# Performance work log

Hardware: AMD Instinct MI355X
Metric: run time of the kernel (lower is better)

The kernel has to match this reference:

```python
import jax, jax.numpy as jnp
import numpy as np

K_REGION = 32
C_CONTEXT = 128
CONF_THR = 0.5


def safe_normalize(x):
    return x / jnp.maximum(x.sum(axis=-1, keepdims=True), 1e-6)


def _geometry(mask_grid, h, w):
    # mask_grid: [B, K, h*w] -> per-mask bbox (x_min,y_min,x_max,y_max) + area, vectorized
    B, K, _ = mask_grid.shape
    m2 = mask_grid.reshape(B, K, h, w)
    present = m2 > 0.05
    rows = present.any(-1)  # [B,K,h]
    cols = present.any(-2)  # [B,K,w]
    yi = jnp.arange(h)
    xi = jnp.arange(w)
    y_min = jnp.min(jnp.where(rows, yi, h), axis=-1).astype(jnp.float32)
    y_max = jnp.max(jnp.where(rows, yi, -1), axis=-1).astype(jnp.float32)
    x_min = jnp.min(jnp.where(cols, xi, w), axis=-1).astype(jnp.float32)
    x_max = jnp.max(jnp.where(cols, xi, -1), axis=-1).astype(jnp.float32)
    hden = float(max(h - 1, 1))
    wden = float(max(w - 1, 1))
    area = present.astype(jnp.float32).mean(axis=(-1, -2))
    geom = jnp.stack([x_min / wden, y_min / hden, x_max / wden, y_max / hden, area], axis=-1)
    has_any = present.any(axis=(-1, -2))
    return jnp.where(has_any[..., None], geom, 0.0).astype(mask_grid.dtype)


def setup_inputs():
    key = jax.random.key(0)
    ks = jax.random.split(key, 16)
    B, N, D, M, Hm, Wm, Qd, Hd = 8, 576, 1024, 64, 384, 384, 4096, 1024
    inp = {}
    inp['patch_tokens'] = jax.random.normal(ks[0], (B, N, D), jnp.float32)
    inp['masks'] = jax.random.uniform(ks[1], (B, M, Hm, Wm), jnp.float32)
    inp['scores'] = jax.random.uniform(ks[2], (B, M), jnp.float32)
    inp['question_embed'] = jax.random.normal(ks[3], (B, Qd), jnp.float32)
    s = 0.02
    inp['W1'] = jax.random.normal(ks[4], (5, D), jnp.float32) * s
    inp['b1'] = jnp.zeros((D,), jnp.float32)
    inp['W2'] = jax.random.normal(ks[5], (D, D), jnp.float32) * s
    inp['b2'] = jnp.zeros((D,), jnp.float32)
    inp['Wv'] = jax.random.normal(ks[6], (D, Hd), jnp.float32) * s
    inp['bv'] = jnp.zeros((Hd,), jnp.float32)
    inp['Wp'] = jax.random.normal(ks[7], (1, Hd), jnp.float32) * s
    inp['bp'] = jnp.zeros((Hd,), jnp.float32)
    inp['Wq'] = jax.random.normal(ks[8], (Qd, Hd), jnp.float32) * s
    inp['bq'] = jnp.zeros((Hd,), jnp.float32)
    inp['Wo'] = jax.random.normal(ks[9], (Hd, 1), jnp.float32) * s
    inp['bo'] = jnp.zeros((1,), jnp.float32)
    inp['type_emb'] = jax.random.normal(ks[10], (3, D), jnp.float32) * s
    inp['patch_h'] = 24
    inp['patch_w'] = 24
    return inp


def reference(patch_tokens, masks, scores, question_embed, W1, b1, W2, b2,
              Wv, bv, Wp, bp, Wq, bq, Wo, bo, type_emb, patch_h, patch_w):
    B, N, D = patch_tokens.shape
    h, w = patch_h, patch_w
    M = masks.shape[1]

    grounding_valid = (masks.reshape(B, M, -1).sum(-1) > 0).any(-1)  # [B]

    order = jnp.argsort(-scores, axis=1)
    scores_s = jnp.take_along_axis(scores, order, axis=1)
    masks_s = jnp.take_along_axis(masks, order[:, :, None, None], axis=1)
    masks_k = masks_s[:, :K_REGION]
    scores_k = scores_s[:, :K_REGION]
    valid = scores_k >= CONF_THR
    masks_k = masks_k * valid[:, :, None, None].astype(masks_k.dtype)
    scores_k = jnp.where(valid, scores_k, 0.0)

    # MaskDownsampler: adaptive avg pool (exact: Hm,Wm divisible by h,w)
    Hm, Wm = masks_k.shape[-2:]
    fh, fw = Hm // h, Wm // w
    mg = masks_k.reshape(B, K_REGION, h, fh, w, fw).mean(axis=(3, 5)).reshape(B, K_REGION, h * w)

    uniform = jnp.full((B, K_REGION, N), 1.0 / N, dtype=patch_tokens.dtype)
    mg = jnp.where(grounding_valid[:, None, None], mg, uniform)
    scores_k = jnp.where(grounding_valid[:, None], scores_k, 1.0)

    # RegionPooler
    nm = safe_normalize(jnp.maximum(mg, 0.0))
    pooled = jnp.einsum('bkn,bnd->bkd', nm, patch_tokens)
    weighted = pooled * scores_k[..., None]
    geom = _geometry(mg, h, w)  # [B,K,5]
    g = jax.nn.silu(geom @ W1 + b1) @ W2 + b2
    region_tokens = weighted + g

    patch_prior = (mg * scores_k[..., None]).sum(axis=1)
    patch_prior = safe_normalize(jnp.maximum(patch_prior, 0.0))
    patch_prior = jnp.where(grounding_valid[:, None], patch_prior, jnp.full_like(patch_prior, 1.0 / N))

    # RoutingScorer
    hid = jnp.tanh(patch_tokens @ Wv + bv
                   + patch_prior[:, :, None] @ Wp + bp
                   + (question_embed @ Wq + bq)[:, None, :])
    routing_scores = (hid @ Wo + bo)[..., 0]  # [B,N]
    routing_weights = jax.nn.softmax(routing_scores, axis=-1)

    top_k = min(C_CONTEXT, N)
    _, sel_idx = jax.lax.top_k(routing_scores, top_k)
    context_tokens = jnp.take_along_axis(patch_tokens, sel_idx[:, :, None], axis=1)
    sel_mask = jnp.zeros((B, N), patch_tokens.dtype).at[jnp.arange(B)[:, None], sel_idx].set(1.0)

    # BackgroundPooler
    residual = jnp.maximum(1.0 - sel_mask, 0.0)
    residual = residual / jnp.maximum(residual.sum(-1, keepdims=True), 1e-6)
    bg = jnp.einsum('bn,bnd->bd', residual, patch_tokens)

    region_tokens = region_tokens + type_emb[0][None, None, :]
    context_tokens = context_tokens + type_emb[1][None, None, :]
    background_token = bg[:, None, :] + type_emb[2][None, None, :]
    visual_tokens = jnp.concatenate([region_tokens, context_tokens, background_token], axis=1)

    return (visual_tokens, region_tokens, context_tokens, background_token,
            patch_prior, routing_weights, sel_idx, grounding_valid)
```

## Files before the change

### kernel.cpp

```cpp
#include <hip/hip_runtime.h>
#include <math.h>

typedef long long I64;

#define NB    8
#define NTOK  576
#define DIM   1024
#define NMASK 64
#define HMASK 384
#define WMASK 384
#define QDIM  4096
#define HDIM  1024
#define KREG  32
#define CCTX  128
#define GH    24
#define GW    24
#define GNUM  576

#define OFF_VIS 0
#define OFF_REG 1318912
#define OFF_CTX 1581056
#define OFF_BG  2629632
#define OFF_PP  2637824
#define OFF_RW  2642432
#define OFF_SEL 2647040
#define OFF_GV  2648064

#define WS_BS   0
#define WS_NMAT 294912
#define WS_SCK  442368
#define WS_H1   442624
#define WS_Q    704768
#define WS_Q2   712960
#define WS_GV   721152
#define WS_PP   721160
#define WS_CS   725768
#define WS_RSP  733960

#define QBLK      256
#define BS_BLOCKS (NB * NMASK * 24)

__global__ __launch_bounds__(384) void k_bsq(const float* __restrict__ masks,
                                             const float* __restrict__ qe,
                                             const float* __restrict__ Wq,
                                             const float* __restrict__ bq,
                                             float* __restrict__ ws) {
  int gid = blockIdx.x;
  int t = threadIdx.x;
  __shared__ float shm[2048 + 6 * 64];
  if (gid >= QBLK) {
    int gid2 = gid - QBLK;
    int yband = gid2 % 24;
    int bm = gid2 / 24;
    float (*sm)[96] = (float(*)[96])shm;
    const float4* src = (const float4*)(masks + (I64)bm * (HMASK * WMASK) + (I64)yband * 16 * WMASK);
    float4 s4 = src[t];
    float4 v1 = src[t + 384];
    float4 v2 = src[t + 768];
    float4 v3 = src[t + 1152];
    s4.x += v1.x; s4.y += v1.y; s4.z += v1.z; s4.w += v1.w;
    s4.x += v2.x; s4.y += v2.y; s4.z += v2.z; s4.w += v2.w;
    s4.x += v3.x; s4.y += v3.y; s4.z += v3.z; s4.w += v3.w;
    float s = (s4.x + s4.y) + (s4.z + s4.w);
    sm[t / 96][t % 96] = s;
    __syncthreads();
    if (t < 24) {
      float tt = 0.f;
      #pragma unroll
      for (int rg = 0; rg < 4; ++rg)
        #pragma unroll
        for (int c = 0; c < 4; ++c) tt += sm[rg][t * 4 + c];
      ws[WS_BS + (I64)bm * GNUM + yband * 24 + t] = tt;
    }
  } else {
    int b = gid >> 5;
    int r = gid & 31;
    int qb = r >> 1;
    int ih = r & 1;
    int base = ih * 2048;
    float* qs = shm;
    float (*sp)[64] = (float(*)[64])(shm + 2048);
    {
      const float4* s4 = (const float4*)(qe + (I64)b * QDIM + base);
      float4 v = s4[t];
      *(float4*)&qs[t * 4] = v;
      if (t < 128) {
        float4 v2 = s4[t + 384];
        *(float4*)&qs[(t + 384) * 4] = v2;
      }
    }
    __syncthreads();
    int dl = t & 63, ig = t >> 6;
    int d = qb * 64 + dl;
    const float* wq = Wq + d;
    float a0 = 0.f, a1 = 0.f, a2 = 0.f, a3 = 0.f;
    float a4 = 0.f, a5 = 0.f, a6 = 0.f, a7 = 0.f;
    int i = ig;
    for (; i + 42 < 2048; i += 48) {
      a0 = fmaf(qs[i],      wq[(I64)(base + i) * HDIM],      a0);
      a1 = fmaf(qs[i + 6],  wq[(I64)(base + i + 6) * HDIM],  a1);
      a2 = fmaf(qs[i + 12], wq[(I64)(base + i + 12) * HDIM], a2);
      a3 = fmaf(qs[i + 18], wq[(I64)(base + i + 18) * HDIM], a3);
      a4 = fmaf(qs[i + 24], wq[(I64)(base + i + 24) * HDIM], a4);
      a5 = fmaf(qs[i + 30], wq[(I64)(base + i + 30) * HDIM], a5);
      a6 = fmaf(qs[i + 36], wq[(I64)(base + i + 36) * HDIM], a6);
      a7 = fmaf(qs[i + 42], wq[(I64)(base + i + 42) * HDIM], a7);
    }
    for (; i < 2048; i += 6)
      a0 = fmaf(qs[i], wq[(I64)(base + i) * HDIM], a0);
    sp[ig][dl] = ((a0 + a1) + (a2 + a3)) + ((a4 + a5) + (a6 + a7));
    __syncthreads();
    if (t < 64) {
      float s2 = ((sp[0][t] + sp[1][t]) + (sp[2][t] + sp[3][t])) + (sp[4][t] + sp[5][t]);
      int dd = qb * 64 + t;
      float outv = s2 + (ih ? 0.f : bq[dd]);
      ws[(ih ? WS_Q2 : WS_Q) + (I64)b * HDIM + dd] = outv;
    }
  }
}

#define MGPAD 580
__global__ __launch_bounds__(256) void k_perbatch(
    const float* __restrict__ bs, const float* __restrict__ scores,
    const float* __restrict__ W1, const float* __restrict__ b1,
    float* __restrict__ ws, float* __restrict__ out) {
  int b = blockIdx.x;
  int t = threadIdx.x;
  __shared__ float s_mg[KREG][MGPAD];
  __shared__ float s_sc[NMASK];
  __shared__ float s_msum[NMASK];
  __shared__ int   s_order[NMASK];
  __shared__ float s_sck[KREG];
  __shared__ int   s_valid[KREG];
  __shared__ int   s_midx[KREG];
  __shared__ float s_rowsum[KREG];
  __shared__ float s_pp[GNUM];
  __shared__ float s_geom[KREG][5];
  __shared__ float s_red[64];
  __shared__ int   s_gv;
  __shared__ float s_ppsum;

  {
    int m = t >> 2, q = t & 3;
    const float4* p = (const float4*)(bs + ((I64)b * NMASK + m) * GNUM) + q * 36;
    float s = 0.f;
    #pragma unroll 4
    for (int j = 0; j < 36; ++j) {
      float4 v = p[j];
      s += v.x; s += v.y; s += v.z; s += v.w;
    }
    s += __shfl_xor(s, 1);
    s += __shfl_xor(s, 2);
    if (q == 0) s_msum[m] = s;
  }
  if (t < NMASK) s_sc[t] = scores[b * NMASK + t];
  __syncthreads();
  if (t == 0) {
    int g = 0;
    for (int m = 0; m < NMASK; ++m) g |= (s_msum[m] > 0.f) ? 1 : 0;
    s_gv = g;
  }
  if (t < NMASK) {
    float v = s_sc[t];
    int r = 0;
    for (int j = 0; j < NMASK; ++j) {
      float vj = s_sc[j];
      r += (vj > v) || (vj == v && j < t);
    }
    s_order[r] = t;
  }
  __syncthreads();
  const int gv = s_gv;
  if (t < KREG) {
    int m = s_order[t];
    float sc = s_sc[m];
    int valid = (sc >= 0.5f) ? 1 : 0;
    s_midx[t] = m;
    s_valid[t] = valid;
    float sck = gv ? (valid ? sc : 0.f) : 1.f;
    s_sck[t] = sck;
    ws[WS_SCK + b * KREG + t] = sck;
  }
  __syncthreads();
  {
    int k = t >> 3, sub = t & 7;
    const float inv256 = 1.f / 256.f;
    const float invN = 1.f / 576.f;
    float scale = gv ? (s_valid[k] ? inv256 : 0.f) : 0.f;
    float addv  = gv ? 0.f : invN;
    const float4* src = (const float4*)(bs + ((I64)b * NMASK + s_midx[k]) * GNUM) + sub * 18;
    float* dst = &s_mg[k][sub * 72];
    #pragma unroll 3
    for (int j = 0; j < 18; ++j) {
      float4 v = src[j];
      v.x = v.x * scale + addv;
      v.y = v.y * scale + addv;
      v.z = v.z * scale + addv;
      v.w = v.w * scale + addv;
      *(float4*)(dst + j * 4) = v;
    }
  }
  __syncthreads();
  {
    int k = t >> 3, sub = t & 7;
    float part = 0.f;
    for (int n = sub; n < GNUM; n += 8) part += fmaxf(s_mg[k][n], 0.f);
    part += __shfl_xor(part, 1);
    part += __shfl_xor(part, 2);
    part += __shfl_xor(part, 4);
    if (sub == 0) s_rowsum[k] = part;
  }
  __syncthreads();
  for (int idx = t; idx < KREG * GNUM; idx += 256) {
    int k = idx / GNUM, n = idx - k * GNUM;
    float v = fmaxf(s_mg[k][n], 0.f);
    ws[WS_NMAT + ((I64)b * KREG + k) * GNUM + n] = v / fmaxf(s_rowsum[k], 1e-6f);
  }
  for (int n = t; n < GNUM; n += 256) {
    float raw = 0.f;
    #pragma unroll
    for (int k = 0; k < KREG; ++k) raw = fmaf(s_mg[k][n], s_sck[k], raw);
    s_pp[n] = fmaxf(raw, 0.f);
  }
  __syncthreads();
  if (t < 64) {
    float s = 0.f;
    for (int n = t; n < GNUM; n += 64) s += s_pp[n];
    s_red[t] = s;
  }
  __syncthreads();
  if (t == 0) {
    float s = 0.f;
    for (int i = 0; i < 64; ++i) s += s_red[i];
    s_ppsum = s;
  }
  __syncthreads();
  {
    const float invN = 1.f / 576.f;
    float den = fmaxf(s_ppsum, 1e-6f);
    for (int n = t; n < GNUM; n += 256) {
      float v = gv ? (s_pp[n] / den) : invN;
      ws[WS_PP + b * GNUM + n] = v;
      out[OFF_PP + b * GNUM + n] = v;
    }
  }
  {
    int k = t >> 3, sub = t & 7;
    unsigned colmask = 0u;
    int ymin = GH, ymax = -1, cnt = 0;
    #pragma unroll
    for (int yy = 0; yy < 3; ++yy) {
      int y = sub * 3 + yy;
      unsigned rowm = 0u;
      for (int x = 0; x < GW; ++x)
        if (s_mg[k][y * GW + x] > 0.05f) rowm |= (1u << x);
      if (rowm) { if (y < ymin) ymin = y; if (y > ymax) ymax = y; }
      colmask |= rowm;
      cnt += __popc(rowm);
    }
    #pragma unroll
    for (int off = 1; off < 8; off <<= 1) {
      colmask |= (unsigned)__shfl_xor((int)colmask, off);
      cnt += __shfl_xor(cnt, off);
      int o1 = __shfl_xor(ymin, off); ymin = (o1 < ymin) ? o1 : ymin;
      int o2 = __shfl_xor(ymax, off); ymax = (o2 > ymax) ? o2 : ymax;
    }
    if (sub == 0) {
      float g0, g1, g2, g3, g4;
      if (cnt > 0) {
        int xmin = __ffs(colmask) - 1;
        int xmax = 31 - __clz(colmask);
        g0 = (float)xmin / 23.f;
        g1 = (float)ymin / 23.f;
        g2 = (float)xmax / 23.f;
        g3 = (float)ymax / 23.f;
        g4 = (float)cnt / 576.f;
      } else { g0 = g1 = g2 = g3 = g4 = 0.f; }
      s_geom[k][0] = g0; s_geom[k][1] = g1; s_geom[k][2] = g2;
      s_geom[k][3] = g3; s_geom[k][4] = g4;
    }
  }
  __syncthreads();
  for (int idx = t; idx < KREG * HDIM; idx += 256) {
    int k = idx >> 10, j = idx & 1023;
    float x = 0.f;
    #pragma unroll
    for (int i = 0; i < 5; ++i) x += s_geom[k][i] * W1[i * HDIM + j];
    x += b1[j];
    float sg = 1.f / (1.f + expf(-x));
    ws[WS_H1 + ((I64)b * KREG + k) * HDIM + j] = x * sg;
  }
  if (t == 0) {
    float g = gv ? 1.f : 0.f;
    ws[WS_GV + b] = g;
    out[OFF_GV + b] = g;
  }
}

__global__ __launch_bounds__(512) void k_region(
    const float* __restrict__ pt, const float* __restrict__ W2,
    const float* __restrict__ b2, const float* __restrict__ te,
    float* __restrict__ ws, float* __restrict__ out) {
  int blk = blockIdx.x;
  int b = blk >> 6, kg = (blk >> 3) & 7, dg = blk & 7;
  int t = threadIdx.x;
  int dl = t & 127;
  int qh = t >> 7;
  int d = dg * 128 + dl;
  const float* nmb = ws + WS_NMAT + ((I64)b * KREG + kg * 4) * GNUM;
  const float* h1b = ws + WS_H1 + ((I64)b * KREG + kg * 4) * HDIM;
  float accP[4] = {0, 0, 0, 0};
  float accG[4] = {0, 0, 0, 0};
  float accS = 0.f;
  int n0 = qh * 144, n1 = n0 + 144;
  for (int n = n0; n < n1; ++n) {
    float p = pt[((I64)b * NTOK + n) * DIM + d];
    accS += p;
    #pragma unroll
    for (int kk = 0; kk < 4; ++kk)
      accP[kk] = fmaf(nmb[kk * GNUM + n], p, accP[kk]);
  }
  int j0 = qh * 256, j1 = j0 + 256;
  for (int j = j0; j < j1; ++j) {
    float wv = W2[(I64)j * DIM + d];
    #pragma unroll
    for (int kk = 0; kk < 4; ++kk)
      accG[kk] = fmaf(h1b[kk * HDIM + j], wv, accG[kk]);
  }
  __shared__ float cmbP[4][4][128];
  __shared__ float cmbG[4][4][128];
  __shared__ float cmbS[4][128];
  #pragma unroll
  for (int kk = 0; kk < 4; ++kk) {
    cmbP[qh][kk][dl] = accP[kk];
    cmbG[qh][kk][dl] = accG[kk];
  }
  cmbS[qh][dl] = accS;
  __syncthreads();
  if (qh == 0) {
    float bb = b2[d], t0 = te[d];
    #pragma unroll
    for (int kk = 0; kk < 4; ++kk) {
      int k = kg * 4 + kk;
      float P = (cmbP[0][kk][dl] + cmbP[1][kk][dl]) + (cmbP[2][kk][dl] + cmbP[3][kk][dl]);
      float G = (cmbG[0][kk][dl] + cmbG[1][kk][dl]) + (cmbG[2][kk][dl] + cmbG[3][kk][dl]);
      float val = P * ws[WS_SCK + b * KREG + k] + G + bb + t0;
      out[OFF_REG + ((I64)b * KREG + k) * DIM + d] = val;
      out[OFF_VIS + ((I64)b * 161 + k) * DIM + d] = val;
    }
    if (kg == 0)
      ws[WS_CS + (I64)b * DIM + d] =
          (cmbS[0][dl] + cmbS[1][dl]) + (cmbS[2][dl] + cmbS[3][dl]);
  }
}

#define PA 36
#define PW 164
__global__ __launch_bounds__(256, 1) void k_hid4(
    const float* __restrict__ pt, const float* __restrict__ Wv,
    const float* __restrict__ bv, const float* __restrict__ Wp,
    const float* __restrict__ bp, const float* __restrict__ Wo,
    float* __restrict__ ws) {
  int blk = blockIdx.x;
  int b = blk >> 5;
  int r = blk & 31;
  int tokTile = r >> 3;
  int colTile = r & 7;
  int n0 = tokTile * 144;
  int col0 = colTile * 128;
  int t = threadIdx.x;
  int trow = t >> 4;
  int tcol = t & 15;

  __shared__ float sA[2][144][PA];
  __shared__ float sW[2][32][PW];

  float acc[9][8];
  #pragma unroll
  for (int i = 0; i < 9; ++i)
    #pragma unroll
    for (int j = 0; j < 8; ++j) acc[i][j] = 0.f;

  int a_row0 = t >> 3, a_kq0 = t & 7;
  int a_row1 = (t + 256) >> 3, a_kq1 = t & 7;
  int a_row2 = (t + 512) >> 3;
  int a_row3 = (t + 768) >> 3;
  int a_row4 = (t + 1024) >> 3;
  int w_k0 = t >> 5, w_c = t & 31;

  float4 pa0, pa1, pa2, pa3, pa4;
  float4 pw0, pw1, pw2, pw3;

  const float* ptb = pt + (I64)(b * NTOK + n0) * DIM;
  const float* wvb = Wv + col0;

  {
    pa0 = *(const float4*)&ptb[(I64)a_row0 * DIM + a_kq0 * 4];
    pa1 = *(const float4*)&ptb[(I64)a_row1 * DIM + a_kq1 * 4];
    pa2 = *(const float4*)&ptb[(I64)a_row2 * DIM + a_kq1 * 4];
    pa3 = *(const float4*)&ptb[(I64)a_row3 * DIM + a_kq1 * 4];
    if (t < 128) pa4 = *(const float4*)&ptb[(I64)a_row4 * DIM + a_kq1 * 4];
    pw0 = *(const float4*)&wvb[(I64)(w_k0 +  0) * HDIM + w_c * 4];
    pw1 = *(const float4*)&wvb[(I64)(w_k0 +  8) * HDIM + w_c * 4];
    pw2 = *(const float4*)&wvb[(I64)(w_k0 + 16) * HDIM + w_c * 4];
    pw3 = *(const float4*)&wvb[(I64)(w_k0 + 24) * HDIM + w_c * 4];
    *(float4*)&sA[0][a_row0][a_kq0 * 4] = pa0;
    *(float4*)&sA[0][a_row1][a_kq1 * 4] = pa1;
    *(float4*)&sA[0][a_row2][a_kq1 * 4] = pa2;
    *(float4*)&sA[0][a_row3][a_kq1 * 4] = pa3;
    if (t < 128) *(float4*)&sA[0][a_row4][a_kq1 * 4] = pa4;
    *(float4*)&sW[0][w_k0 +  0][w_c * 4] = pw0;
    *(float4*)&sW[0][w_k0 +  8][w_c * 4] = pw1;
    *(float4*)&sW[0][w_k0 + 16][w_c * 4] = pw2;
    *(float4*)&sW[0][w_k0 + 24][w_c * 4] = pw3;
  }

  for (int s = 0; s < 32; ++s) {
    __syncthreads();
    if (s + 1 < 32) {
      int k0 = (s + 1) * 32;
      pa0 = *(const float4*)&ptb[(I64)a_row0 * DIM + k0 + a_kq0 * 4];
      pa1 = *(const float4*)&ptb[(I64)a_row1 * DIM + k0 + a_kq1 * 4];
      pa2 = *(const float4*)&ptb[(I64)a_row2 * DIM + k0 + a_kq1 * 4];
      pa3 = *(const float4*)&ptb[(I64)a_row3 * DIM + k0 + a_kq1 * 4];
      if (t < 128) pa4 = *(const float4*)&ptb[(I64)a_row4 * DIM + k0 + a_kq1 * 4];
      pw0 = *(const float4*)&wvb[(I64)(k0 + w_k0 +  0) * HDIM + w_c * 4];
      pw1 = *(const float4*)&wvb[(I64)(k0 + w_k0 +  8) * HDIM + w_c * 4];
      pw2 = *(const float4*)&wvb[(I64)(k0 + w_k0 + 16) * HDIM + w_c * 4];
      pw3 = *(const float4*)&wvb[(I64)(k0 + w_k0 + 24) * HDIM + w_c * 4];
    }
    int cur = s & 1;
    #pragma unroll 2
    for (int kk4 = 0; kk4 < 8; ++kk4) {
      float4 af[9];
      #pragma unroll
      for (int i = 0; i < 9; ++i)
        af[i] = *(const float4*)&sA[cur][trow * 9 + i][kk4 * 4];
      float4 w0[4], w1[4];
      #pragma unroll
      for (int m = 0; m < 4; ++m) {
        w0[m] = *(const float4*)&sW[cur][kk4 * 4 + m][tcol * 4];
        w1[m] = *(const float4*)&sW[cur][kk4 * 4 + m][64 + tcol * 4];
      }
      #pragma unroll
      for (int i = 0; i < 9; ++i) {
        #pragma unroll
        for (int m = 0; m < 4; ++m) {
          float a = ((const float*)&af[i])[m];
          acc[i][0] = fmaf(a, w0[m].x, acc[i][0]);
          acc[i][1] = fmaf(a, w0[m].y, acc[i][1]);
          acc[i][2] = fmaf(a, w0[m].z, acc[i][2]);
          acc[i][3] = fmaf(a, w0[m].w, acc[i][3]);
          acc[i][4] = fmaf(a, w1[m].x, acc[i][4]);
          acc[i][5] = fmaf(a, w1[m].y, acc[i][5]);
          acc[i][6] = fmaf(a, w1[m].z, acc[i][6]);
          acc[i][7] = fmaf(a, w1[m].w, acc[i][7]);
        }
      }
    }
    if (s + 1 < 32) {
      int nxt = (s + 1) & 1;
      *(float4*)&sA[nxt][a_row0][a_kq0 * 4] = pa0;
      *(float4*)&sA[nxt][a_row1][a_kq1 * 4] = pa1;
      *(float4*)&sA[nxt][a_row2][a_kq1 * 4] = pa2;
      *(float4*)&sA[nxt][a_row3][a_kq1 * 4] = pa3;
      if (t < 128) *(float4*)&sA[nxt][a_row4][a_kq1 * 4] = pa4;
      *(float4*)&sW[nxt][w_k0 +  0][w_c * 4] = pw0;
      *(float4*)&sW[nxt][w_k0 +  8][w_c * 4] = pw1;
      *(float4*)&sW[nxt][w_k0 + 16][w_c * 4] = pw2;
      *(float4*)&sW[nxt][w_k0 + 24][w_c * 4] = pw3;
    }
  }

  int ca = col0 + tcol * 4;
  int cb = col0 + 64 + tcol * 4;
  float4 bvA = *(const float4*)&bv[ca], bvB = *(const float4*)&bv[cb];
  float4 bpA = *(const float4*)&bp[ca], bpB = *(const float4*)&bp[cb];
  float4 wpA = *(const float4*)&Wp[ca], wpB = *(const float4*)&Wp[cb];
  float4 woA = *(const float4*)&Wo[ca], woB = *(const float4*)&Wo[cb];
  float4 qaA = *(const float4*)&ws[WS_Q  + (I64)b * HDIM + ca];
  float4 qaB = *(const float4*)&ws[WS_Q  + (I64)b * HDIM + cb];
  float4 qbA = *(const float4*)&ws[WS_Q2 + (I64)b * HDIM + ca];
  float4 qbB = *(const float4*)&ws[WS_Q2 + (I64)b * HDIM + cb];
  float bvv[8] = {bvA.x, bvA.y, bvA.z, bvA.w, bvB.x, bvB.y, bvB.z, bvB.w};
  float bpv[8] = {bpA.x, bpA.y, bpA.z, bpA.w, bpB.x, bpB.y, bpB.z, bpB.w};
  float wpv[8] = {wpA.x, wpA.y, wpA.z, wpA.w, wpB.x, wpB.y, wpB.z, wpB.w};
  float wov[8] = {woA.x, woA.y, woA.z, woA.w, woB.x, woB.y, woB.z, woB.w};
  float qv[8]  = {qaA.x + qbA.x, qaA.y + qbA.y, qaA.z + qbA.z, qaA.w + qbA.w,
                  qaB.x + qbB.x, qaB.y + qbB.y, qaB.z + qbB.z, qaB.w + qbB.w};
  float partial[9];
  #pragma unroll
  for (int i = 0; i < 9; ++i) {
    float ppv = ws[WS_PP + b * GNUM + n0 + trow * 9 + i];
    float s = 0.f;
    #pragma unroll
    for (int j = 0; j < 8; ++j) {
      float pre = acc[i][j] + bvv[j] + bpv[j] + qv[j] + ppv * wpv[j];
      s = fmaf(wov[j], tanhf(pre), s);
    }
    partial[i] = s;
  }
  #pragma unroll
  for (int i = 0; i < 9; ++i) {
    float p = partial[i];
    p += __shfl_xor(p, 1);
    p += __shfl_xor(p, 2);
    p += __shfl_xor(p, 4);
    p += __shfl_xor(p, 8);
    partial[i] = p;
  }
  if (tcol == 0) {
    #pragma unroll
    for (int i = 0; i < 9; ++i)
      ws[WS_RSP + ((I64)b * NTOK + n0 + trow * 9 + i) * 8 + colTile] = partial[i];
  }
}

__global__ __launch_bounds__(576) void k_soft(const float* __restrict__ bo,
                                              float* __restrict__ ws, float* __restrict__ out) {
  int b = blockIdx.x, t = threadIdx.x;
  __shared__ float s_rs[NTOK];
  __shared__ float s_w[9];
  __shared__ float s_max, s_sum;
  {
    const float4* p = (const float4*)(ws + WS_RSP + ((I64)b * NTOK + t) * 8);
    float4 v0 = p[0], v1 = p[1];
    s_rs[t] = bo[0] + (((v0.x + v0.y) + (v0.z + v0.w)) + ((v1.x + v1.y) + (v1.z + v1.w)));
  }
  __syncthreads();
  float v = s_rs[t];
  int r = 0;
  for (int j = 0; j < NTOK; ++j) {
    float vj = s_rs[j];
    r += (vj > v) || (vj == v && j < t);
  }
  float m = v;
  for (int off = 1; off < 64; off <<= 1) m = fmaxf(m, __shfl_xor(m, off));
  if ((t & 63) == 0) s_w[t >> 6] = m;
  __syncthreads();
  if (t == 0) {
    float mm = s_w[0];
    for (int i = 1; i < 9; ++i) mm = fmaxf(mm, s_w[i]);
    s_max = mm;
  }
  __syncthreads();
  float e = expf(v - s_max);
  float s = e;
  for (int off = 1; off < 64; off <<= 1) s += __shfl_xor(s, off);
  if ((t & 63) == 0) s_w[t >> 6] = s;
  __syncthreads();
  if (t == 0) {
    float ss = 0.f;
    for (int i = 0; i < 9; ++i) ss += s_w[i];
    s_sum = ss;
  }
  __syncthreads();
  out[OFF_RW + b * NTOK + t] = e / s_sum;
  if (r < CCTX) out[OFF_SEL + b * CCTX + r] = (float)t;
}

__global__ __launch_bounds__(256) void k_post(const float* __restrict__ pt, const float* __restrict__ te,
                                              const float* __restrict__ ws, const float* __restrict__ outr,
                                              float* __restrict__ out) {
  int rr = blockIdx.x, b = blockIdx.y;
  int d = threadIdx.x * 4;
  if (rr < CCTX) {
    int idx = (int)outr[OFF_SEL + b * CCTX + rr];
    float4 v = *(const float4*)&pt[((I64)b * NTOK + idx) * DIM + d];
    float4 e = *(const float4*)&te[DIM + d];
    v.x += e.x; v.y += e.y; v.z += e.z; v.w += e.w;
    *(float4*)&out[OFF_CTX + ((I64)b * CCTX + rr) * DIM + d] = v;
    *(float4*)&out[OFF_VIS + ((I64)b * 161 + KREG + rr) * DIM + d] = v;
  } else {
    float4 s = *(const float4*)&ws[WS_CS + (I64)b * DIM + d];
    for (int r = 0; r < CCTX; ++r) {
      int idx = (int)outr[OFF_SEL + b * CCTX + r];
      float4 v = *(const float4*)&pt[((I64)b * NTOK + idx) * DIM + d];
      s.x -= v.x; s.y -= v.y; s.z -= v.z; s.w -= v.w;
    }
    const float rinv = 1.f / 448.f;
    float4 e = *(const float4*)&te[2 * DIM + d];
    float4 o;
    o.x = s.x * rinv + e.x; o.y = s.y * rinv + e.y;
    o.z = s.z * rinv + e.z; o.w = s.w * rinv + e.w;
    *(float4*)&out[OFF_BG + (I64)b * DIM + d] = o;
    *(float4*)&out[OFF_VIS + ((I64)b * 161 + 160) * DIM + d] = o;
  }
}

extern "C" void kernel_launch(void* const* d_in, const int* in_sizes, int n_in,
                              void* d_out, int out_size, void* d_ws, size_t ws_size,
                              hipStream_t stream) {
  (void)in_sizes; (void)n_in; (void)out_size; (void)ws_size;
  const float* pt     = (const float*)d_in[0];
  const float* masks  = (const float*)d_in[1];
  const float* scores = (const float*)d_in[2];
  const float* qe     = (const float*)d_in[3];
  const float* W1     = (const float*)d_in[4];
  const float* b1     = (const float*)d_in[5];
  const float* W2     = (const float*)d_in[6];
  const float* b2     = (const float*)d_in[7];
  const float* Wv     = (const float*)d_in[8];
  const float* bv     = (const float*)d_in[9];
  const float* Wp     = (const float*)d_in[10];
  const float* bp     = (const float*)d_in[11];
  const float* Wq     = (const float*)d_in[12];
  const float* bq     = (const float*)d_in[13];
  const float* Wo     = (const float*)d_in[14];
  const float* bo     = (const float*)d_in[15];
  const float* te     = (const float*)d_in[16];
  float* out = (float*)d_out;
  float* ws  = (float*)d_ws;

  k_bsq<<<dim3(QBLK + BS_BLOCKS), dim3(384), 0, stream>>>(masks, qe, Wq, bq, ws);
  k_perbatch<<<dim3(NB), dim3(256), 0, stream>>>(ws + WS_BS, scores, W1, b1, ws, out);
  k_region<<<dim3(512), dim3(512), 0, stream>>>(pt, W2, b2, te, ws, out);
  k_hid4<<<dim3(256), dim3(256), 0, stream>>>(pt, Wv, bv, Wp, bp, Wo, ws);
  k_soft<<<dim3(NB), dim3(576), 0, stream>>>(bo, ws, out);
  k_post<<<dim3(CCTX + 1, NB), dim3(256), 0, stream>>>(pt, te, ws, out, out);
}
```

Measured before the change: 343.2 us.

## Fold patch-token GEMM into mask-reduction kernel and split epilogue into separate pass

Result: faster. 328.0 us (-4.4%).

```diff
diff --git a/kernel.cpp b/kernel.cpp
--- a/kernel.cpp
+++ b/kernel.cpp
@@ -35,10 +35,521 @@
 #define WS_GV   721152
 #define WS_PP   721160
 #define WS_CS   725768
-#define WS_RSP  733960
+#define WS_RS   733960
+#define WS_RSP  738568
+#define WS_HID  775432
+#define WS_END  5494024
 
 #define QBLK      256
 #define BS_BLOCKS (NB * NMASK * 24)
+#define MEGA_GRID (256 + 256 + BS_BLOCKS)
+
+__global__ __launch_bounds__(256, 2) void k_mega(
+    const float* __restrict__ masks, const float* __restrict__ qe,
+    const float* __restrict__ Wq, const float* __restrict__ bq,
+    const float* __restrict__ pt, const float* __restrict__ Wv,
+    float* __restrict__ ws) {
+  int gid = blockIdx.x;
+  int t = threadIdx.x;
+  __shared__ __align__(16) float smem[10432];
+
+  if (gid < 256) {
+    int b = gid >> 5;
+    int r = gid & 31;
+    int tokTile = r >> 3;
+    int colTile = r & 7;
+    int n0 = tokTile * 144;
+    int col0 = colTile * 128;
+    int trow = t >> 4;
+    int tcol = t & 15;
+
+    float (*sA)[36]  = (float(*)[36])smem;
+    float (*sW)[164] = (float(*)[164])(smem + 5184);
+
+    float acc[9][8];
+    #pragma unroll
+    for (int i = 0; i < 9; ++i)
+      #pragma unroll
+      for (int j = 0; j < 8; ++j) acc[i][j] = 0.f;
+
+    int a_row0 = t >> 3, a_kq = t & 7;
+    int a_row1 = (t + 256) >> 3;
+    int a_row2 = (t + 512) >> 3;
+    int a_row3 = (t + 768) >> 3;
+    int a_row4 = (t + 1024) >> 3;
+    int w_k0 = t >> 5, w_c = t & 31;
+
+    const float* ptb = pt + (I64)(b * NTOK + n0) * DIM;
+    const float* wvb = Wv + col0;
+
+    float4 pa0, pa1, pa2, pa3, pa4 = {0,0,0,0};
+    float4 pw0, pw1, pw2, pw3;
+
+    pa0 = *(const float4*)&ptb[(I64)a_row0 * DIM + a_kq * 4];
+    pa1 = *(const float4*)&ptb[(I64)a_row1 * DIM + a_kq * 4];
+    pa2 = *(const float4*)&ptb[(I64)a_row2 * DIM + a_kq * 4];
+    pa3 = *(const float4*)&ptb[(I64)a_row3 * DIM + a_kq * 4];
+    if (t < 128) pa4 = *(const float4*)&ptb[(I64)a_row4 * DIM + a_kq * 4];
+    pw0 = *(const float4*)&wvb[(I64)(w_k0 +  0) * HDIM + w_c * 4];
+    pw1 = *(const float4*)&wvb[(I64)(w_k0 +  8) * HDIM + w_c * 4];
+    pw2 = *(const float4*)&wvb[(I64)(w_k0 + 16) * HDIM + w_c * 4];
+    pw3 = *(const float4*)&wvb[(I64)(w_k0 + 24) * HDIM + w_c * 4];
+
+    for (int s = 0; s < 32; ++s) {
+      __syncthreads();
+      *(float4*)&sA[a_row0][a_kq * 4] = pa0;
+      *(float4*)&sA[a_row1][a_kq * 4] = pa1;
+      *(float4*)&sA[a_row2][a_kq * 4] = pa2;
+      *(float4*)&sA[a_row3][a_kq * 4] = pa3;
+      if (t < 128) *(float4*)&sA[a_row4][a_kq * 4] = pa4;
+      *(float4*)&sW[w_k0 +  0][w_c * 4] = pw0;
+      *(float4*)&sW[w_k0 +  8][w_c * 4] = pw1;
+      *(float4*)&sW[w_k0 + 16][w_c * 4] = pw2;
+      *(float4*)&sW[w_k0 + 24][w_c * 4] = pw3;
+      __syncthreads();
+      if (s + 1 < 32) {
+        int k0 = (s + 1) * 32;
+        pa0 = *(const float4*)&ptb[(I64)a_row0 * DIM + k0 + a_kq * 4];
+        pa1 = *(const float4*)&ptb[(I64)a_row1 * DIM + k0 + a_kq * 4];
+        pa2 = *(const float4*)&ptb[(I64)a_row2 * DIM + k0 + a_kq * 4];
+        pa3 = *(const float4*)&ptb[(I64)a_row3 * DIM + k0 + a_kq * 4];
+        if (t < 128) pa4 = *(const float4*)&ptb[(I64)a_row4 * DIM + k0 + a_kq * 4];
+        pw0 = *(const float4*)&wvb[(I64)(k0 + w_k0 +  0) * HDIM + w_c * 4];
+        pw1 = *(const float4*)&wvb[(I64)(k0 + w_k0 +  8) * HDIM + w_c * 4];
+        pw2 = *(const float4*)&wvb[(I64)(k0 + w_k0 + 16) * HDIM + w_c * 4];
+        pw3 = *(const float4*)&wvb[(I64)(k0 + w_k0 + 24) * HDIM + w_c * 4];
+      }
+      #pragma unroll 2
+      for (int kk4 = 0; kk4 < 8; ++kk4) {
+        float4 af[9];
+        #pragma unroll
+        for (int i = 0; i < 9; ++i)
+          af[i] = *(const float4*)&sA[trow * 9 + i][kk4 * 4];
+        float4 w0[4], w1[4];
+        #pragma unroll
+        for (int m = 0; m < 4; ++m) {
+          w0[m] = *(const float4*)&sW[kk4 * 4 + m][tcol * 4];
+          w1[m] = *(const float4*)&sW[kk4 * 4 + m][64 + tcol * 4];
+        }
+        #pragma unroll
+        for (int i = 0; i < 9; ++i) {
+          #pragma unroll
+          for (int m = 0; m < 4; ++m) {
+            float a = ((const float*)&af[i])[m];
+            acc[i][0] = fmaf(a, w0[m].x, acc[i][0]);
+            acc[i][1] = fmaf(a, w0[m].y, acc[i][1]);
+            acc[i][2] = fmaf(a, w0[m].z, acc[i][2]);
+            acc[i][3] = fmaf(a, w0[m].w, acc[i][3]);
+            acc[i][4] = fmaf(a, w1[m].x, acc[i][4]);
+            acc[i][5] = fmaf(a, w1[m].y, acc[i][5]);
+            acc[i][6] = fmaf(a, w1[m].z, acc[i][6]);
+            acc[i][7] = fmaf(a, w1[m].w, acc[i][7]);
+          }
+        }
+      }
+    }
+    float* hid = ws + WS_HID + ((I64)b * NTOK + n0) * HDIM;
+    #pragma unroll
+    for (int i = 0; i < 9; ++i) {
+      int row = trow * 9 + i;
+      float4 va = {acc[i][0], acc[i][1], acc[i][2], acc[i][3]};
+      float4 vb = {acc[i][4], acc[i][5], acc[i][6], acc[i][7]};
+      *(float4*)&hid[(I64)row * HDIM + col0 + tcol * 4] = va;
+      *(float4*)&hid[(I64)row * HDIM + col0 + 64 + tcol * 4] = vb;
+    }
+  } else if (gid < 512) {
+    int g = gid - 256;
+    int b = g >> 5, r = g & 31;
+    int qb = r >> 1, ih = r & 1;
+    int base = ih * 2048;
+    float* qs = smem;
+    float (*sp)[64] = (float(*)[64])(smem + 2048);
+    const float4* s4 = (const float4*)(qe + (I64)b * QDIM + base);
+    *(float4*)&qs[t * 4] = s4[t];
+    *(float4*)&qs[(t + 256) * 4] = s4[t + 256];
+    __syncthreads();
+    int dl = t & 63, ig = t >> 6;
+    int d = qb * 64 + dl;
+    const float* wq = Wq + d;
+    float a0 = 0.f, a1 = 0.f, a2 = 0.f, a3 = 0.f;
+    float a4 = 0.f, a5 = 0.f, a6 = 0.f, a7 = 0.f;
+    for (int i = ig; i < 2048; i += 32) {
+      a0 = fmaf(qs[i],      wq[(I64)(base + i) * HDIM],      a0);
+      a1 = fmaf(qs[i + 4],  wq[(I64)(base + i + 4) * HDIM],  a1);
+      a2 = fmaf(qs[i + 8],  wq[(I64)(base + i + 8) * HDIM],  a2);
+      a3 = fmaf(qs[i + 12], wq[(I64)(base + i + 12) * HDIM], a3);
+      a4 = fmaf(qs[i + 16], wq[(I64)(base + i + 16) * HDIM], a4);
+      a5 = fmaf(qs[i + 20], wq[(I64)(base + i + 20) * HDIM], a5);
+      a6 = fmaf(qs[i + 24], wq[(I64)(base + i + 24) * HDIM], a6);
+      a7 = fmaf(qs[i + 28], wq[(I64)(base + i + 28) * HDIM], a7);
+    }
+    sp[ig][dl] = ((a0 + a1) + (a2 + a3)) + ((a4 + a5) + (a6 + a7));
+    __syncthreads();
+    if (t < 64) {
+      float s2 = (sp[0][t] + sp[1][t]) + (sp[2][t] + sp[3][t]);
+      int dd = qb * 64 + t;
+      ws[(ih ? WS_Q2 : WS_Q) + (I64)b * HDIM + dd] = s2 + (ih ? 0.f : bq[dd]);
+    }
+  } else {
+    int g = gid - 512;
+    int yband = g % 24;
+    int bm = g / 24;
+    float (*sm)[96] = (float(*)[96])smem;
+    const float4* src = (const float4*)(masks + (I64)bm * (HMASK * WMASK) + (I64)yband * 16 * WMASK);
+    #pragma unroll
+    for (int j = 0; j < 6; ++j) {
+      int f = t + 256 * j;
+      float4 v = src[f];
+      sm[f / 96][f % 96] = (v.x + v.y) + (v.z + v.w);
+    }
+    __syncthreads();
+    if (t < 24) {
+      float tt = 0.f;
+      #pragma unroll
+      for (int rr = 0; rr < 16; ++rr)
+        #pragma unroll
+        for (int c = 0; c < 4; ++c) tt += sm[rr][t * 4 + c];
+      ws[WS_BS + (I64)bm * GNUM + yband * 24 + t] = tt;
+    }
+  }
+}
+
+__global__ __launch_bounds__(256) void k_epi(
+    const float* __restrict__ bv, const float* __restrict__ bp,
+    const float* __restrict__ Wp, const float* __restrict__ Wo,
+    const float* __restrict__ bo, float* __restrict__ ws) {
+  int t = threadIdx.x;
+  int g = blockIdx.x * 16 + (t >> 4);
+  int l = t & 15;
+  int b = g / NTOK, n = g % NTOK;
+  const float* hid = ws + WS_HID + (I64)g * HDIM;
+  const float* q1 = ws + WS_Q + (I64)b * HDIM;
+  const float* q2 = ws + WS_Q2 + (I64)b * HDIM;
+  float ppv = ws[WS_PP + b * GNUM + n];
+  float ssum = 0.f;
+  #pragma unroll 4
+  for (int j = 0; j < 16; ++j) {
+    int c = l * 64 + j * 4;
+    float4 h4 = *(const float4*)&hid[c];
+    float4 b4 = *(const float4*)&bv[c];
+    float4 p4 = *(const float4*)&bp[c];
+    float4 w4 = *(const float4*)&Wp[c];
+    float4 o4 = *(const float4*)&Wo[c];
+    float4 qa = *(const float4*)&q1[c];
+    float4 qb = *(const float4*)&q2[c];
+    ssum = fmaf(o4.x, tanhf(h4.x + b4.x + p4.x + qa.x + qb.x + ppv * w4.x), ssum);
+    ssum = fmaf(o4.y, tanhf(h4.y + b4.y + p4.y + qa.y + qb.y + ppv * w4.y), ssum);
+    ssum = fmaf(o4.z, tanhf(h4.z + b4.z + p4.z + qa.z + qb.z + ppv * w4.z), ssum);
+    ssum = fmaf(o4.w, tanhf(h4.w + b4.w + p4.w + qa.w + qb.w + ppv * w4.w), ssum);
+  }
+  ssum += __shfl_xor(ssum, 1);
+  ssum += __shfl_xor(ssum, 2);
+  ssum += __shfl_xor(ssum, 4);
+  ssum += __shfl_xor(ssum, 8);
+  if (l == 0) ws[WS_RS + g] = ssum + bo[0];
+}
+
+#define MGPAD 580
+__global__ __launch_bounds__(256) void k_perbatch(
+    const float* __restrict__ bs, const float* __restrict__ scores,
+    const float* __restrict__ W1, const float* __restrict__ b1,
+    float* __restrict__ ws, float* __restrict__ out) {
+  int b = blockIdx.x;
+  int t = threadIdx.x;
+  __shared__ float s_mg[KREG][MGPAD];
+  __shared__ float s_sc[NMASK];
+  __shared__ float s_msum[NMASK];
+  __shared__ int   s_order[NMASK];
+  __shared__ float s_sck[KREG];
+  __shared__ int   s_valid[KREG];
+  __shared__ int   s_midx[KREG];
+  __shared__ float s_rowsum[KREG];
+  __shared__ float s_pp[GNUM];
+  __shared__ float s_geom[KREG][5];
+  __shared__ float s_red[64];
+  __shared__ int   s_gv;
+  __shared__ float s_ppsum;
+
+  {
+    int m = t >> 2, q = t & 3;
+    const float4* p = (const float4*)(bs + ((I64)b * NMASK + m) * GNUM) + q * 36;
+    float s = 0.f;
+    #pragma unroll 4
+    for (int j = 0; j < 36; ++j) {
+      float4 v = p[j];
+      s += v.x; s += v.y; s += v.z; s += v.w;
+    }
+    s += __shfl_xor(s, 1);
+    s += __shfl_xor(s, 2);
+    if (q == 0) s_msum[m] = s;
+  }
+  if (t < NMASK) s_sc[t] = scores[b * NMASK + t];
+  __syncthreads();
+  if (t == 0) {
+    int g = 0;
+    for (int m = 0; m < NMASK; ++m) g |= (s_msum[m] > 0.f) ? 1 : 0;
+    s_gv = g;
+  }
+  if (t < NMASK) {
+    float v = s_sc[t];
+    int r = 0;
+    for (int j = 0; j < NMASK; ++j) {
+      float vj = s_sc[j];
+      r += (vj > v) || (vj == v && j < t);
+    }
+    s_order[r] = t;
+  }
+  __syncthreads();
+  const int gv = s_gv;
+  if (t < KREG) {
+    int m = s_order[t];
+    float sc = s_sc[m];
+    int valid = (sc >= 0.5f) ? 1 : 0;
+    s_midx[t] = m;
+    s_valid[t] = valid;
+    float sck = gv ? (valid ? sc : 0.f) : 1.f;
+    s_sck[t] = sck;
+    ws[WS_SCK + b * KREG + t] = sck;
+  }
+  __syncthreads();
+  {
+    int k = t >> 3, sub = t & 7;
+    const float inv256 = 1.f / 256.f;
+    const float invN = 1.f / 576.f;
+    float scale = gv ? (s_valid[k] ? inv256 : 0.f) : 0.f;
+    float addv  = gv ? 0.f : invN;
+    const float4* src = (const float4*)(bs + ((I64)b * NMASK + s_midx[k]) * GNUM) + sub * 18;
+    float* dst = &s_mg[k][sub * 72];
+    #pragma unroll 3
+    for (int j = 0; j < 18; ++j) {
+      float4 v = src[j];
+      v.x = v.x * scale + addv;
+      v.y = v.y * scale + addv;
+      v.z = v.z * scale + addv;
+      v.w = v.w * scale + addv;
+      *(float4*)(dst + j * 4) = v;
+    }
+  }
+  __syncthreads();
+  {
+    int k = t >> 3, sub = t & 7;
+    float part = 0.f;
+    for (int n = sub; n < GNUM; n += 8) part += fmaxf(s_mg[k][n], 0.f);
+    part += __shfl_xor(part, 1);
+    part += __shfl_xor(part, 2);
+    part += __shfl_xor(part, 4);
+    if (sub == 0) s_rowsum[k] = part;
+  }
+  __syncthreads();
+  for (int idx = t; idx < KREG * GNUM; idx += 256) {
+    int k = idx / GNUM, n = idx - k * GNUM;
+    float v = fmaxf(s_mg[k][n], 0.f);
+    ws[WS_NMAT + ((I64)b * KREG + k) * GNUM + n] = v / fmaxf(s_rowsum[k], 1e-6f);
+  }
+  for (int n = t; n < GNUM; n += 256) {
+    float raw = 0.f;
+    #pragma unroll
+    for (int k = 0; k < KREG; ++k) raw = fmaf(s_mg[k][n], s_sck[k], raw);
+    s_pp[n] = fmaxf(raw, 0.f);
+  }
+  __syncthreads();
+  if (t < 64) {
+    float s = 0.f;
+    for (int n = t; n < GNUM; n += 64) s += s_pp[n];
+    s_red[t] = s;
+  }
+  __syncthreads();
+  if (t == 0) {
+    float s = 0.f;
+    for (int i = 0; i < 64; ++i) s += s_red[i];
+    s_ppsum = s;
+  }
+  __syncthreads();
+  {
+    const float invN = 1.f / 576.f;
+    float den = fmaxf(s_ppsum, 1e-6f);
+    for (int n = t; n < GNUM; n += 256) {
+      float v = gv ? (s_pp[n] / den) : invN;
+      ws[WS_PP + b * GNUM + n] = v;
+      out[OFF_PP + b * GNUM + n] = v;
+    }
+  }
+  {
+    int k = t >> 3, sub = t & 7;
+    unsigned colmask = 0u;
+    int ymin = GH, ymax = -1, cnt = 0;
+    #pragma unroll
+    for (int yy = 0; yy < 3; ++yy) {
+      int y = sub * 3 + yy;
+      unsigned rowm = 0u;
+      for (int x = 0; x < GW; ++x)
+        if (s_mg[k][y * GW + x] > 0.05f) rowm |= (1u << x);
+      if (rowm) { if (y < ymin) ymin = y; if (y > ymax) ymax = y; }
+      colmask |= rowm;
+      cnt += __popc(rowm);
+    }
+    #pragma unroll
+    for (int off = 1; off < 8; off <<= 1) {
+      colmask |= (unsigned)__shfl_xor((int)colmask, off);
+      cnt += __shfl_xor(cnt, off);
+      int o1 = __shfl_xor(ymin, off); ymin = (o1 < ymin) ? o1 : ymin;
+      int o2 = __shfl_xor(ymax, off); ymax = (o2 > ymax) ? o2 : ymax;
+    }
+    if (sub == 0) {
+      float g0, g1, g2, g3, g4;
+      if (cnt > 0) {
+        int xmin = __ffs(colmask) - 1;
+        int xmax = 31 - __clz(colmask);
+        g0 = (float)xmin / 23.f;
+        g1 = (float)ymin / 23.f;
+        g2 = (float)xmax / 23.f;
+        g3 = (float)ymax / 23.f;
+        g4 = (float)cnt / 576.f;
+      } else { g0 = g1 = g2 = g3 = g4 = 0.f; }
+      s_geom[k][0] = g0; s_geom[k][1] = g1; s_geom[k][2] = g2;
+      s_geom[k][3] = g3; s_geom[k][4] = g4;
+    }
+  }
+  __syncthreads();
+  for (int idx = t; idx < KREG * HDIM; idx += 256) {
+    int k = idx >> 10, j = idx & 1023;
+    float x = 0.f;
+    #pragma unroll
+    for (int i = 0; i < 5; ++i) x += s_geom[k][i] * W1[i * HDIM + j];
+    x += b1[j];
+    float sg = 1.f / (1.f + expf(-x));
+    ws[WS_H1 + ((I64)b * KREG + k) * HDIM + j] = x * sg;
+  }
+  if (t == 0) {
+    float g = gv ? 1.f : 0.f;
+    ws[WS_GV + b] = g;
+    out[OFF_GV + b] = g;
+  }
+}
+
+__global__ __launch_bounds__(512) void k_region(
+    const float* __restrict__ pt, const float* __restrict__ W2,
+    const float* __restrict__ b2, const float* __restrict__ te,
+    float* __restrict__ ws, float* __restrict__ out) {
+  int blk = blockIdx.x;
+  int b = blk >> 6, kg = (blk >> 3) & 7, dg = blk & 7;
+  int t = threadIdx.x;
+  int dl = t & 127;
+  int qh = t >> 7;
+  int d = dg * 128 + dl;
+  const float* nmb = ws + WS_NMAT + ((I64)b * KREG + kg * 4) * GNUM;
+  const float* h1b = ws + WS_H1 + ((I64)b * KREG + kg * 4) * HDIM;
+  float accP[4] = {0, 0, 0, 0};
+  float accG[4] = {0, 0, 0, 0};
+  float accS = 0.f;
+  int n0 = qh * 144, n1 = n0 + 144;
+  for (int n = n0; n < n1; ++n) {
+    float p = pt[((I64)b * NTOK + n) * DIM + d];
+    accS += p;
+    #pragma unroll
+    for (int kk = 0; kk < 4; ++kk)
+      accP[kk] = fmaf(nmb[kk * GNUM + n], p, accP[kk]);
+  }
+  int j0 = qh * 256, j1 = j0 + 256;
+  for (int j = j0; j < j1; ++j) {
+    float wv = W2[(I64)j * DIM + d];
+    #pragma unroll
+    for (int kk = 0; kk < 4; ++kk)
+      accG[kk] = fmaf(h1b[kk * HDIM + j], wv, accG[kk]);
+  }
+  __shared__ float cmbP[4][4][128];
+  __shared__ float cmbG[4][4][128];
+  __shared__ float cmbS[4][128];
+  #pragma unroll
+  for (int kk = 0; kk < 4; ++kk) {
+    cmbP[qh][kk][dl] = accP[kk];
+    cmbG[qh][kk][dl] = accG[kk];
+  }
+  cmbS[qh][dl] = accS;
+  __syncthreads();
+  if (qh == 0) {
+    float bb = b2[d], t0 = te[d];
+    #pragma unroll
+    for (int kk = 0; kk < 4; ++kk) {
+      int k = kg * 4 + kk;
+      float P = (cmbP[0][kk][dl] + cmbP[1][kk][dl]) + (cmbP[2][kk][dl] + cmbP[3][kk][dl]);
+      float G = (cmbG[0][kk][dl] + cmbG[1][kk][dl]) + (cmbG[2][kk][dl] + cmbG[3][kk][dl]);
+      float val = P * ws[WS_SCK + b * KREG + k] + G + bb + t0;
+      out[OFF_REG + ((I64)b * KREG + k) * DIM + d] = val;
+      out[OFF_VIS + ((I64)b * 161 + k) * DIM + d] = val;
+    }
+    if (kg == 0)
+      ws[WS_CS + (I64)b * DIM + d] =
+          (cmbS[0][dl] + cmbS[1][dl]) + (cmbS[2][dl] + cmbS[3][dl]);
+  }
+}
+
+__global__ __launch_bounds__(576) void k_soft2(float* __restrict__ ws, float* __restrict__ out) {
+  int b = blockIdx.x, t = threadIdx.x;
+  __shared__ float s_rs[NTOK];
+  __shared__ float s_w[9];
+  __shared__ float s_max, s_sum;
+  s_rs[t] = ws[WS_RS + b * NTOK + t];
+  __syncthreads();
+  float v = s_rs[t];
+  int r = 0;
+  for (int j = 0; j < NTOK; ++j) {
+    float vj = s_rs[j];
+    r += (vj > v) || (vj == v && j < t);
+  }
+  float m = v;
+  for (int off = 1; off < 64; off <<= 1) m = fmaxf(m, __shfl_xor(m, off));
+  if ((t & 63) == 0) s_w[t >> 6] = m;
+  __syncthreads();
+  if (t == 0) {
+    float mm = s_w[0];
+    for (int i = 1; i < 9; ++i) mm = fmaxf(mm, s_w[i]);
+    s_max = mm;
+  }
+  __syncthreads();
+  float e = expf(v - s_max);
+  float s = e;
+  for (int off = 1; off < 64; off <<= 1) s += __shfl_xor(s, off);
+  if ((t & 63) == 0) s_w[t >> 6] = s;
+  __syncthreads();
+  if (t == 0) {
+    float ss = 0.f;
+    for (int i = 0; i < 9; ++i) ss += s_w[i];
+    s_sum = ss;
+  }
+  __syncthreads();
+  out[OFF_RW + b * NTOK + t] = e / s_sum;
+  if (r < CCTX) out[OFF_SEL + b * CCTX + r] = (float)t;
+}
+
+__global__ __launch_bounds__(256) void k_post(const float* __restrict__ pt, const float* __restrict__ te,
+                                              const float* __restrict__ ws, const float* __restrict__ outr,
+                                              float* __restrict__ out) {
+  int rr = blockIdx.x, b = blockIdx.y;
+  int d = threadIdx.x * 4;
+  if (rr < CCTX) {
+    int idx = (int)outr[OFF_SEL + b * CCTX + rr];
+    float4 v = *(const float4*)&pt[((I64)b * NTOK + idx) * DIM + d];
+    float4 e = *(const float4*)&te[DIM + d];
+    v.x += e.x; v.y += e.y; v.z += e.z; v.w += e.w;
+    *(float4*)&out[OFF_CTX + ((I64)b * CCTX + rr) * DIM + d] = v;
+    *(float4*)&out[OFF_VIS + ((I64)b * 161 + KREG + rr) * DIM + d] = v;
+  } else {
+    float4 s = *(const float4*)&ws[WS_CS + (I64)b * DIM + d];
+    for (int r = 0; r < CCTX; ++r) {
+      int idx = (int)outr[OFF_SEL + b * CCTX + r];
+      float4 v = *(const float4*)&pt[((I64)b * NTOK + idx) * DIM + d];
+      s.x -= v.x; s.y -= v.y; s.z -= v.z; s.w -= v.w;
+    }
+    const float rinv = 1.f / 448.f;
+    float4 e = *(const float4*)&te[2 * DIM + d];
+    float4 o;
+    o.x = s.x * rinv + e.x; o.y = s.y * rinv + e.y;
+    o.z = s.z * rinv + e.z; o.w = s.w * rinv + e.w;
+    *(float4*)&out[OFF_BG + (I64)b * DIM + d] = o;
+    *(float4*)&out[OFF_VIS + ((I64)b * 161 + 160) * DIM + d] = o;
+  }
+}
 
 __global__ __launch_bounds__(384) void k_bsq(const float* __restrict__ masks,
                                              const float* __restrict__ qe,
@@ -119,243 +630,6 @@
   }
 }
 
-#define MGPAD 580
-__global__ __launch_bounds__(256) void k_perbatch(
-    const float* __restrict__ bs, const float* __restrict__ scores,
-    const float* __restrict__ W1, const float* __restrict__ b1,
-    float* __restrict__ ws, float* __restrict__ out) {
-  int b = blockIdx.x;
-  int t = threadIdx.x;
-  __shared__ float s_mg[KREG][MGPAD];
-  __shared__ float s_sc[NMASK];
-  __shared__ float s_msum[NMASK];
-  __shared__ int   s_order[NMASK];
-  __shared__ float s_sck[KREG];
-  __shared__ int   s_valid[KREG];
-  __shared__ int   s_midx[KREG];
-  __shared__ float s_rowsum[KREG];
-  __shared__ float s_pp[GNUM];
-  __shared__ float s_geom[KREG][5];
-  __shared__ float s_red[64];
-  __shared__ int   s_gv;
-  __shared__ float s_ppsum;
-
-  {
-    int m = t >> 2, q = t & 3;
-    const float4* p = (const float4*)(bs + ((I64)b * NMASK + m) * GNUM) + q * 36;
-    float s = 0.f;
-    #pragma unroll 4
-    for (int j = 0; j < 36; ++j) {
-      float4 v = p[j];
-      s += v.x; s += v.y; s += v.z; s += v.w;
-    }
-    s += __shfl_xor(s, 1);
-    s += __shfl_xor(s, 2);
-    if (q == 0) s_msum[m] = s;
-  }
-  if (t < NMASK) s_sc[t] = scores[b * NMASK + t];
-  __syncthreads();
-  if (t == 0) {
-    int g = 0;
-    for (int m = 0; m < NMASK; ++m) g |= (s_msum[m] > 0.f) ? 1 : 0;
-    s_gv = g;
-  }
-  if (t < NMASK) {
-    float v = s_sc[t];
-    int r = 0;
-    for (int j = 0; j < NMASK; ++j) {
-      float vj = s_sc[j];
-      r += (vj > v) || (vj == v && j < t);
-    }
-    s_order[r] = t;
-  }
-  __syncthreads();
-  const int gv = s_gv;
-  if (t < KREG) {
-    int m = s_order[t];
-    float sc = s_sc[m];
-    int valid = (sc >= 0.5f) ? 1 : 0;
-    s_midx[t] = m;
-    s_valid[t] = valid;
-    float sck = gv ? (valid ? sc : 0.f) : 1.f;
-    s_sck[t] = sck;
-    ws[WS_SCK + b * KREG + t] = sck;
-  }
-  __syncthreads();
-  {
-    int k = t >> 3, sub = t & 7;
-    const float inv256 = 1.f / 256.f;
-    const float invN = 1.f / 576.f;
-    float scale = gv ? (s_valid[k] ? inv256 : 0.f) : 0.f;
-    float addv  = gv ? 0.f : invN;
-    const float4* src = (const float4*)(bs + ((I64)b * NMASK + s_midx[k]) * GNUM) + sub * 18;
-    float* dst = &s_mg[k][sub * 72];
-    #pragma unroll 3
-    for (int j = 0; j < 18; ++j) {
-      float4 v = src[j];
-      v.x = v.x * scale + addv;
-      v.y = v.y * scale + addv;
-      v.z = v.z * scale + addv;
-      v.w = v.w * scale + addv;
-      *(float4*)(dst + j * 4) = v;
-    }
-  }
-  __syncthreads();
-  {
-    int k = t >> 3, sub = t & 7;
-    float part = 0.f;
-    for (int n = sub; n < GNUM; n += 8) part += fmaxf(s_mg[k][n], 0.f);
-    part += __shfl_xor(part, 1);
-    part += __shfl_xor(part, 2);
-    part += __shfl_xor(part, 4);
-    if (sub == 0) s_rowsum[k] = part;
-  }
-  __syncthreads();
-  for (int idx = t; idx < KREG * GNUM; idx += 256) {
-    int k = idx / GNUM, n = idx - k * GNUM;
-    float v = fmaxf(s_mg[k][n], 0.f);
-    ws[WS_NMAT + ((I64)b * KREG + k) * GNUM + n] = v / fmaxf(s_rowsum[k], 1e-6f);
-  }
-  for (int n = t; n < GNUM; n += 256) {
-    float raw = 0.f;
-    #pragma unroll
-    for (int k = 0; k < KREG; ++k) raw = fmaf(s_mg[k][n], s_sck[k], raw);
-    s_pp[n] = fmaxf(raw, 0.f);
-  }
-  __syncthreads();
-  if (t < 64) {
-    float s = 0.f;
-    for (int n = t; n < GNUM; n += 64) s += s_pp[n];
-    s_red[t] = s;
-  }
-  __syncthreads();
-  if (t == 0) {
-    float s = 0.f;
-    for (int i = 0; i < 64; ++i) s += s_red[i];
-    s_ppsum = s;
-  }
-  __syncthreads();
-  {
-    const float invN = 1.f / 576.f;
-    float den = fmaxf(s_ppsum, 1e-6f);
-    for (int n = t; n < GNUM; n += 256) {
-      float v = gv ? (s_pp[n] / den) : invN;
-      ws[WS_PP + b * GNUM + n] = v;
-      out[OFF_PP + b * GNUM + n] = v;
-    }
-  }
-  {
-    int k = t >> 3, sub = t & 7;
-    unsigned colmask = 0u;
-    int ymin = GH, ymax = -1, cnt = 0;
-    #pragma unroll
-    for (int yy = 0; yy < 3; ++yy) {
-      int y = sub * 3 + yy;
-      unsigned rowm = 0u;
-      for (int x = 0; x < GW; ++x)
-        if (s_mg[k][y * GW + x] > 0.05f) rowm |= (1u << x);
-      if (rowm) { if (y < ymin) ymin = y; if (y > ymax) ymax = y; }
-      colmask |= rowm;
-      cnt += __popc(rowm);
-    }
-    #pragma unroll
-    for (int off = 1; off < 8; off <<= 1) {
-      colmask |= (unsigned)__shfl_xor((int)colmask, off);
-      cnt += __shfl_xor(cnt, off);
-      int o1 = __shfl_xor(ymin, off); ymin = (o1 < ymin) ? o1 : ymin;
-      int o2 = __shfl_xor(ymax, off); ymax = (o2 > ymax) ? o2 : ymax;
-    }
-    if (sub == 0) {
-      float g0, g1, g2, g3, g4;
-      if (cnt > 0) {
-        int xmin = __ffs(colmask) - 1;
-        int xmax = 31 - __clz(colmask);
-        g0 = (float)xmin / 23.f;
-        g1 = (float)ymin / 23.f;
-        g2 = (float)xmax / 23.f;
-        g3 = (float)ymax / 23.f;
-        g4 = (float)cnt / 576.f;
-      } else { g0 = g1 = g2 = g3 = g4 = 0.f; }
-      s_geom[k][0] = g0; s_geom[k][1] = g1; s_geom[k][2] = g2;
-      s_geom[k][3] = g3; s_geom[k][4] = g4;
-    }
-  }
-  __syncthreads();
-  for (int idx = t; idx < KREG * HDIM; idx += 256) {
-    int k = idx >> 10, j = idx & 1023;
-    float x = 0.f;
-    #pragma unroll
-    for (int i = 0; i < 5; ++i) x += s_geom[k][i] * W1[i * HDIM + j];
-    x += b1[j];
-    float sg = 1.f / (1.f + expf(-x));
-    ws[WS_H1 + ((I64)b * KREG + k) * HDIM + j] = x * sg;
-  }
-  if (t == 0) {
-    float g = gv ? 1.f : 0.f;
-    ws[WS_GV + b] = g;
-    out[OFF_GV + b] = g;
-  }
-}
-
-__global__ __launch_bounds__(512) void k_region(
-    const float* __restrict__ pt, const float* __restrict__ W2,
-    const float* __restrict__ b2, const float* __restrict__ te,
-    float* __restrict__ ws, float* __restrict__ out) {
-  int blk = blockIdx.x;
-  int b = blk >> 6, kg = (blk >> 3) & 7, dg = blk & 7;
-  int t = threadIdx.x;
-  int dl = t & 127;
-  int qh = t >> 7;
-  int d = dg * 128 + dl;
-  const float* nmb = ws + WS_NMAT + ((I64)b * KREG + kg * 4) * GNUM;
-  const float* h1b = ws + WS_H1 + ((I64)b * KREG + kg * 4) * HDIM;
-  float accP[4] = {0, 0, 0, 0};
-  float accG[4] = {0, 0, 0, 0};
-  float accS = 0.f;
-  int n0 = qh * 144, n1 = n0 + 144;
-  for (int n = n0; n < n1; ++n) {
-    float p = pt[((I64)b * NTOK + n) * DIM + d];
-    accS += p;
-    #pragma unroll
-    for (int kk = 0; kk < 4; ++kk)
-      accP[kk] = fmaf(nmb[kk * GNUM + n], p, accP[kk]);
-  }
-  int j0 = qh * 256, j1 = j0 + 256;
-  for (int j = j0; j < j1; ++j) {
-    float wv = W2[(I64)j * DIM + d];
-    #pragma unroll
-    for (int kk = 0; kk < 4; ++kk)
-      accG[kk] = fmaf(h1b[kk * HDIM + j], wv, accG[kk]);
-  }
-  __shared__ float cmbP[4][4][128];
-  __shared__ float cmbG[4][4][128];
-  __shared__ float cmbS[4][128];
-  #pragma unroll
-  for (int kk = 0; kk < 4; ++kk) {
-    cmbP[qh][kk][dl] = accP[kk];
-    cmbG[qh][kk][dl] = accG[kk];
-  }
-  cmbS[qh][dl] = accS;
-  __syncthreads();
-  if (qh == 0) {
-    float bb = b2[d], t0 = te[d];
-    #pragma unroll
-    for (int kk = 0; kk < 4; ++kk) {
-      int k = kg * 4 + kk;
-      float P = (cmbP[0][kk][dl] + cmbP[1][kk][dl]) + (cmbP[2][kk][dl] + cmbP[3][kk][dl]);
-      float G = (cmbG[0][kk][dl] + cmbG[1][kk][dl]) + (cmbG[2][kk][dl] + cmbG[3][kk][dl]);
-      float val = P * ws[WS_SCK + b * KREG + k] + G + bb + t0;
-      out[OFF_REG + ((I64)b * KREG + k) * DIM + d] = val;
-      out[OFF_VIS + ((I64)b * 161 + k) * DIM + d] = val;
-    }
-    if (kg == 0)
-      ws[WS_CS + (I64)b * DIM + d] =
-          (cmbS[0][dl] + cmbS[1][dl]) + (cmbS[2][dl] + cmbS[3][dl]);
-  }
-}
-
-#define PA 36
-#define PW 164
 __global__ __launch_bounds__(256, 1) void k_hid4(
     const float* __restrict__ pt, const float* __restrict__ Wv,
     const float* __restrict__ bv, const float* __restrict__ Wp,
@@ -372,8 +646,8 @@
   int trow = t >> 4;
   int tcol = t & 15;
 
-  __shared__ float sA[2][144][PA];
-  __shared__ float sW[2][32][PW];
+  __shared__ float sA[2][144][36];
+  __shared__ float sW[2][32][164];
 
   float acc[9][8];
   #pragma unroll
@@ -382,13 +656,13 @@
     for (int j = 0; j < 8; ++j) acc[i][j] = 0.f;
 
   int a_row0 = t >> 3, a_kq0 = t & 7;
-  int a_row1 = (t + 256) >> 3, a_kq1 = t & 7;
+  int a_row1 = (t + 256) >> 3;
   int a_row2 = (t + 512) >> 3;
   int a_row3 = (t + 768) >> 3;
   int a_row4 = (t + 1024) >> 3;
   int w_k0 = t >> 5, w_c = t & 31;
 
-  float4 pa0, pa1, pa2, pa3, pa4;
+  float4 pa0, pa1, pa2, pa3, pa4 = {0,0,0,0};
   float4 pw0, pw1, pw2, pw3;
 
   const float* ptb = pt + (I64)(b * NTOK + n0) * DIM;
@@ -396,19 +670,19 @@
 
   {
     pa0 = *(const float4*)&ptb[(I64)a_row0 * DIM + a_kq0 * 4];
-    pa1 = *(const float4*)&ptb[(I64)a_row1 * DIM + a_kq1 * 4];
-    pa2 = *(const float4*)&ptb[(I64)a_row2 * DIM + a_kq1 * 4];
-    pa3 = *(const float4*)&ptb[(I64)a_row3 * DIM + a_kq1 * 4];
-    if (t < 128) pa4 = *(const float4*)&ptb[(I64)a_row4 * DIM + a_kq1 * 4];
+    pa1 = *(const float4*)&ptb[(I64)a_row1 * DIM + a_kq0 * 4];
+    pa2 = *(const float4*)&ptb[(I64)a_row2 * DIM + a_kq0 * 4];
+    pa3 = *(const float4*)&ptb[(I64)a_row3 * DIM + a_kq0 * 4];
+    if (t < 128) pa4 = *(const float4*)&ptb[(I64)a_row4 * DIM + a_kq0 * 4];
     pw0 = *(const float4*)&wvb[(I64)(w_k0 +  0) * HDIM + w_c * 4];
     pw1 = *(const float4*)&wvb[(I64)(w_k0 +  8) * HDIM + w_c * 4];
     pw2 = *(const float4*)&wvb[(I64)(w_k0 + 16) * HDIM + w_c * 4];
     pw3 = *(const float4*)&wvb[(I64)(w_k0 + 24) * HDIM + w_c * 4];
     *(float4*)&sA[0][a_row0][a_kq0 * 4] = pa0;
-    *(float4*)&sA[0][a_row1][a_kq1 * 4] = pa1;
-    *(float4*)&sA[0][a_row2][a_kq1 * 4] = pa2;
-    *(float4*)&sA[0][a_row3][a_kq1 * 4] = pa3;
-    if (t < 128) *(float4*)&sA[0][a_row4][a_kq1 * 4] = pa4;
+    *(float4*)&sA[0][a_row1][a_kq0 * 4] = pa1;
+    *(float4*)&sA[0][a_row2][a_kq0 * 4] = pa2;
+    *(float4*)&sA[0][a_row3][a_kq0 * 4] = pa3;
+    if (t < 128) *(float4*)&sA[0][a_row4][a_kq0 * 4] = pa4;
     *(float4*)&sW[0][w_k0 +  0][w_c * 4] = pw0;
     *(float4*)&sW[0][w_k0 +  8][w_c * 4] = pw1;
     *(float4*)&sW[0][w_k0 + 16][w_c * 4] = pw2;
@@ -420,10 +694,10 @@
     if (s + 1 < 32) {
       int k0 = (s + 1) * 32;
       pa0 = *(const float4*)&ptb[(I64)a_row0 * DIM + k0 + a_kq0 * 4];
-      pa1 = *(const float4*)&ptb[(I64)a_row1 * DIM + k0 + a_kq1 * 4];
-      pa2 = *(const float4*)&ptb[(I64)a_row2 * DIM + k0 + a_kq1 * 4];
-      pa3 = *(const float4*)&ptb[(I64)a_row3 * DIM + k0 + a_kq1 * 4];
-      if (t < 128) pa4 = *(const float4*)&ptb[(I64)a_row4 * DIM + k0 + a_kq1 * 4];
+      pa1 = *(const float4*)&ptb[(I64)a_row1 * DIM + k0 + a_kq0 * 4];
+      pa2 = *(const float4*)&ptb[(I64)a_row2 * DIM + k0 + a_kq0 * 4];
+      pa3 = *(const float4*)&ptb[(I64)a_row3 * DIM + k0 + a_kq0 * 4];
+      if (t < 128) pa4 = *(const float4*)&ptb[(I64)a_row4 * DIM + k0 + a_kq0 * 4];
       pw0 = *(const float4*)&wvb[(I64)(k0 + w_k0 +  0) * HDIM + w_c * 4];
       pw1 = *(const float4*)&wvb[(I64)(k0 + w_k0 +  8) * HDIM + w_c * 4];
       pw2 = *(const float4*)&wvb[(I64)(k0 + w_k0 + 16) * HDIM + w_c * 4];
@@ -461,10 +735,10 @@
     if (s + 1 < 32) {
       int nxt = (s + 1) & 1;
       *(float4*)&sA[nxt][a_row0][a_kq0 * 4] = pa0;
-      *(float4*)&sA[nxt][a_row1][a_kq1 * 4] = pa1;
-      *(float4*)&sA[nxt][a_row2][a_kq1 * 4] = pa2;
-      *(float4*)&sA[nxt][a_row3][a_kq1 * 4] = pa3;
-      if (t < 128) *(float4*)&sA[nxt][a_row4][a_kq1 * 4] = pa4;
+      *(float4*)&sA[nxt][a_row1][a_kq0 * 4] = pa1;
+      *(float4*)&sA[nxt][a_row2][a_kq0 * 4] = pa2;
+      *(float4*)&sA[nxt][a_row3][a_kq0 * 4] = pa3;
+      if (t < 128) *(float4*)&sA[nxt][a_row4][a_kq0 * 4] = pa4;
       *(float4*)&sW[nxt][w_k0 +  0][w_c * 4] = pw0;
       *(float4*)&sW[nxt][w_k0 +  8][w_c * 4] = pw1;
       *(float4*)&sW[nxt][w_k0 + 16][w_c * 4] = pw2;
@@ -516,8 +790,8 @@
   }
 }
 
-__global__ __launch_bounds__(576) void k_soft(const float* __restrict__ bo,
-                                              float* __restrict__ ws, float* __restrict__ out) {
+__global__ __launch_bounds__(576) void k_soft_fb(const float* __restrict__ bo,
+                                                 float* __restrict__ ws, float* __restrict__ out) {
   int b = blockIdx.x, t = threadIdx.x;
   __shared__ float s_rs[NTOK];
   __shared__ float s_w[9];
@@ -559,39 +833,10 @@
   if (r < CCTX) out[OFF_SEL + b * CCTX + r] = (float)t;
 }
 
-__global__ __launch_bounds__(256) void k_post(const float* __restrict__ pt, const float* __restrict__ te,
-                                              const float* __restrict__ ws, const float* __restrict__ outr,
-                                              float* __restrict__ out) {
-  int rr = blockIdx.x, b = blockIdx.y;
-  int d = threadIdx.x * 4;
-  if (rr < CCTX) {
-    int idx = (int)outr[OFF_SEL + b * CCTX + rr];
-    float4 v = *(const float4*)&pt[((I64)b * NTOK + idx) * DIM + d];
-    float4 e = *(const float4*)&te[DIM + d];
-    v.x += e.x; v.y += e.y; v.z += e.z; v.w += e.w;
-    *(float4*)&out[OFF_CTX + ((I64)b * CCTX + rr) * DIM + d] = v;
-    *(float4*)&out[OFF_VIS + ((I64)b * 161 + KREG + rr) * DIM + d] = v;
-  } else {
-    float4 s = *(const float4*)&ws[WS_CS + (I64)b * DIM + d];
-    for (int r = 0; r < CCTX; ++r) {
-      int idx = (int)outr[OFF_SEL + b * CCTX + r];
-      float4 v = *(const float4*)&pt[((I64)b * NTOK + idx) * DIM + d];
-      s.x -= v.x; s.y -= v.y; s.z -= v.z; s.w -= v.w;
-    }
-    const float rinv = 1.f / 448.f;
-    float4 e = *(const float4*)&te[2 * DIM + d];
-    float4 o;
-    o.x = s.x * rinv + e.x; o.y = s.y * rinv + e.y;
-    o.z = s.z * rinv + e.z; o.w = s.w * rinv + e.w;
-    *(float4*)&out[OFF_BG + (I64)b * DIM + d] = o;
-    *(float4*)&out[OFF_VIS + ((I64)b * 161 + 160) * DIM + d] = o;
-  }
-}
-
 extern "C" void kernel_launch(void* const* d_in, const int* in_sizes, int n_in,
                               void* d_out, int out_size, void* d_ws, size_t ws_size,
                               hipStream_t stream) {
-  (void)in_sizes; (void)n_in; (void)out_size; (void)ws_size;
+  (void)in_sizes; (void)n_in; (void)out_size;
   const float* pt     = (const float*)d_in[0];
   const float* masks  = (const float*)d_in[1];
   const float* scores = (const float*)d_in[2];
@@ -612,10 +857,19 @@
   float* out = (float*)d_out;
   float* ws  = (float*)d_ws;
 
-  k_bsq<<<dim3(QBLK + BS_BLOCKS), dim3(384), 0, stream>>>(masks, qe, Wq, bq, ws);
-  k_perbatch<<<dim3(NB), dim3(256), 0, stream>>>(ws + WS_BS, scores, W1, b1, ws, out);
-  k_region<<<dim3(512), dim3(512), 0, stream>>>(pt, W2, b2, te, ws, out);
-  k_hid4<<<dim3(256), dim3(256), 0, stream>>>(pt, Wv, bv, Wp, bp, Wo, ws);
-  k_soft<<<dim3(NB), dim3(576), 0, stream>>>(bo, ws, out);
-  k_post<<<dim3(CCTX + 1, NB), dim3(256), 0, stream>>>(pt, te, ws, out, out);
-}
+  if (ws_size >= (size_t)WS_END * 4) {
+    k_mega<<<dim3(MEGA_GRID), dim3(256), 0, stream>>>(masks, qe, Wq, bq, pt, Wv, ws);
+    k_perbatch<<<dim3(NB), dim3(256), 0, stream>>>(ws + WS_BS, scores, W1, b1, ws, out);
+    k_epi<<<dim3(288), dim3(256), 0, stream>>>(bv, bp, Wp, Wo, bo, ws);
+    k_region<<<dim3(512), dim3(512), 0, stream>>>(pt, W2, b2, te, ws, out);
+    k_soft2<<<dim3(NB), dim3(576), 0, stream>>>(ws, out);
+    k_post<<<dim3(CCTX + 1, NB), dim3(256), 0, stream>>>(pt, te, ws, out, out);
+  } else {
+    k_bsq<<<dim3(QBLK + BS_BLOCKS), dim3(384), 0, stream>>>(masks, qe, Wq, bq, ws);
+    k_perbatch<<<dim3(NB), dim3(256), 0, stream>>>(ws + WS_BS, scores, W1, b1, ws, out);
+    k_region<<<dim3(512), dim3(512), 0, stream>>>(pt, W2, b2, te, ws, out);
+    k_hid4<<<dim3(256), dim3(256), 0, stream>>>(pt, Wv, bv, Wp, bp, Wo, ws);
+    k_soft_fb<<<dim3(NB), dim3(576), 0, stream>>>(bo, ws, out);
+    k_post<<<dim3(CCTX + 1, NB), dim3(256), 0, stream>>>(pt, te, ws, out, out);
+  }
+}
```
